# Kernel tuning notes

Hardware: AMD Instinct MI355X
Metric: run time of the kernel (lower is better)

Reference implementation:

```python
import jax, jax.numpy as jnp
import numpy as np

B, N, D = 4, 2048, 1024
H = 16
HD = D // H          # 64
SCALE = 1.0 / HD     # module uses 1/head_dim (NOT 1/sqrt)
NEG = -10000.0       # masked_fill value used by the module
THETA = 10000.0


def setup_inputs() -> dict:
    key = jax.random.key(0)
    ks = jax.random.split(key, 6)
    s = (1.0 / D) ** 0.5  # init_method_normal((1/dim)**0.5)
    return {
        "x": jax.random.normal(ks[0], (B, N, D), jnp.float32),
        "Wq": jax.random.normal(ks[1], (D, D), jnp.float32) * s,
        "Wk": jax.random.normal(ks[2], (D, D), jnp.float32) * s,
        "Wv": jax.random.normal(ks[3], (D, D), jnp.float32) * s,
        "Wo": jax.random.normal(ks[4], (D, D), jnp.float32) * s,
        "bo": jnp.zeros((D,), jnp.float32),
    }


def _rope(t):
    # t: [b, h, n, d]; interleaved-pair rotary (lucidrains rotate_queries_or_keys)
    d, n = t.shape[-1], t.shape[-2]
    inv_freq = 1.0 / (THETA ** (jnp.arange(0, d, 2, dtype=jnp.float32) / d))  # [d/2]
    ang = jnp.arange(n, dtype=jnp.float32)[:, None] * inv_freq[None, :]        # [n, d/2]
    cos = jnp.repeat(jnp.cos(ang), 2, axis=-1)  # [n, d]
    sin = jnp.repeat(jnp.sin(ang), 2, axis=-1)
    x1, x2 = t[..., ::2], t[..., 1::2]
    rot = jnp.stack([-x2, x1], axis=-1).reshape(t.shape)  # rotate_half
    return t * cos + rot * sin


def reference(x, Wq, Wk, Wv, Wo, bo):
    b, n, _ = x.shape
    # QKV projections (no bias; torch Linear: x @ W.T)
    q = (x @ Wq.T).reshape(b, n, H, HD).transpose(0, 2, 1, 3)  # [b,h,n,d]
    k = (x @ Wk.T).reshape(b, n, H, HD).transpose(0, 2, 1, 3)
    v = (x @ Wv.T).reshape(b, n, H, HD).transpose(0, 2, 1, 3)
    # RoPE on q, k
    q = _rope(q)
    k = _rope(k)
    # additive mask: 0 on/below diagonal, -10000 above (causal_mask=True path)
    i = jnp.arange(n)
    add_mask = jnp.where(i[:, None] >= i[None, :], 0.0, NEG).astype(x.dtype)  # [n,n]
    scores = jnp.einsum("bhqd,bhkd->bhqk", q, k) * SCALE + add_mask
    attn = jax.nn.softmax(scores, axis=-1)
    out = jnp.einsum("bhqk,bhkd->bhqd", attn, v)            # [b,h,n,d]
    out = out.transpose(0, 2, 1, 3).reshape(b, n, H * HD)    # [b,n,D]
    return out @ Wo.T + bo
```

## Files before the change

### kernel.cpp

```cpp
#include <hip/hip_runtime.h>
#include <hip/hip_bf16.h>
#include <math.h>

#define B_ 4
#define N_ 2048
#define D_ 1024
#define H_ 16
#define HD_ 64
#define SCALE_ 0.015625f
#define MD_ ((size_t)B_ * N_ * D_)
#define DD_ ((size_t)D_ * D_)
#define BHSZ_ ((size_t)N_ * HD_)
#define QSC_ 0.0225421143f

typedef __hip_bfloat16 bf16;
typedef __attribute__((ext_vector_type(8))) __bf16 bf16x8;
typedef __attribute__((ext_vector_type(4))) float f32x4;
typedef __attribute__((ext_vector_type(16))) float f32x16;

__device__ __forceinline__ float b2f(bf16 x) { return __bfloat162float(x); }
__device__ __forceinline__ bf16 f2b(float x) { return __float2bfloat16(x); }

__device__ __forceinline__ unsigned int pk2(float a, float b) {
  union { bf16 h[2]; unsigned int u; } t;
  t.h[0] = f2b(a); t.h[1] = f2b(b);
  return t.u;
}
__device__ __forceinline__ unsigned int pk2t(float a, float b) {
  return (__float_as_uint(a) >> 16) | (__float_as_uint(b) & 0xffff0000u);
}

__device__ __forceinline__ void gl_lds16(const bf16* g, bf16* l) {
  __builtin_amdgcn_global_load_lds(
      (const __attribute__((address_space(1))) void*)g,
      (__attribute__((address_space(3))) void*)l, 16, 0, 0);
}

__global__ __launch_bounds__(256) void cvt_all(
    const float* __restrict__ x,  const float* __restrict__ wq,
    const float* __restrict__ wk, const float* __restrict__ wv,
    const float* __restrict__ wo, bf16* __restrict__ xb,
    bf16* __restrict__ wb)
{
  const int blk = blockIdx.x;
  const float* s; bf16* d; int i;
  if (blk < 4096)      { s = x;  d = xb;           i = blk; }
  else if (blk < 4608) { s = wq; d = wb;           i = blk - 4096; }
  else if (blk < 5120) { s = wk; d = wb + DD_;     i = blk - 4608; }
  else if (blk < 5632) { s = wv; d = wb + 2 * DD_; i = blk - 5120; }
  else                 { s = wo; d = wb + 3 * DD_; i = blk - 5632; }
  int e = (i * 256 + threadIdx.x) * 8;
  float4 a = *reinterpret_cast<const float4*>(s + e);
  float4 b = *reinterpret_cast<const float4*>(s + e + 4);
  bf16 t[8] = {f2b(a.x), f2b(a.y), f2b(a.z), f2b(a.w),
               f2b(b.x), f2b(b.y), f2b(b.z), f2b(b.w)};
  *reinterpret_cast<int4*>(d + e) = *reinterpret_cast<const int4*>(t);
}

template <int MODE>
__global__ __launch_bounds__(256) void mgemm(
    const bf16* __restrict__ A, const bf16* __restrict__ W,
    const float* __restrict__ bias, void* __restrict__ Cv,
    int M, int N, int K)
{
  __shared__ bf16 As[128 * 32];
  __shared__ bf16 Ws[128 * 32];

  const int tid  = threadIdx.x;
  const int w    = tid >> 6;
  const int lane = tid & 63;
  const int bm   = blockIdx.y * 128;
  const int bn   = blockIdx.x * 128;

  const int wr = (w >> 1) * 64;
  const int wc = (w & 1) * 64;
  const int lm   = lane & 15;
  const int quad = lane >> 4;

  const int srow = lane >> 2;
  const int sslot = (lane & 3) ^ ((lane >> 3) & 3);
  const int scol = sslot * 8;

  const int rsw  = (quad ^ ((lm >> 1) & 3)) * 8;

  f32x4 acc[4][4] = {};

  for (int k0 = 0; k0 < K; k0 += 32) {
#pragma unroll
    for (int cc = 0; cc < 2; ++cc) {
      int c = w * 2 + cc;
      int r = c * 16 + srow;
      gl_lds16(A + (size_t)(bm + r) * K + k0 + scol, &As[c * 512]);
      gl_lds16(W + (size_t)(bn + r) * K + k0 + scol, &Ws[c * 512]);
    }
    __syncthreads();

    bf16x8 af[4], bf_[4];
#pragma unroll
    for (int mi = 0; mi < 4; ++mi)
      af[mi] = *reinterpret_cast<const bf16x8*>(&As[(wr + mi * 16 + lm) * 32 + rsw]);
#pragma unroll
    for (int ni = 0; ni < 4; ++ni)
      bf_[ni] = *reinterpret_cast<const bf16x8*>(&Ws[(wc + ni * 16 + lm) * 32 + rsw]);

#pragma unroll
    for (int mi = 0; mi < 4; ++mi)
#pragma unroll
      for (int ni = 0; ni < 4; ++ni)
        acc[mi][ni] = __builtin_amdgcn_mfma_f32_16x16x32_bf16(
            af[mi], bf_[ni], acc[mi][ni], 0, 0, 0);
    __syncthreads();
  }

#pragma unroll
  for (int mi = 0; mi < 4; ++mi) {
#pragma unroll
    for (int r = 0; r < 4; ++r) {
      int row = bm + wr + mi * 16 + quad * 4 + r;
#pragma unroll
      for (int ni = 0; ni < 4; ++ni) {
        int col = bn + wc + ni * 16 + lm;
        float v = acc[mi][ni][r];
        if (MODE == 1) {
          v += bias[col];
          reinterpret_cast<float*>(Cv)[(size_t)row * N + col] = v;
        } else {
          int reg = col >> 10;
          int cc  = col & 1023;
          int bb  = row >> 11;
          int n   = row & (N_ - 1);
          int hh  = cc >> 6;
          int dd  = cc & 63;
          if (reg < 2) {
            int t32 = n >> 5, m = n & 31;
            int s = dd >> 4, hb = (dd >> 3) & 1, j = dd & 7;
            reinterpret_cast<bf16*>(Cv)[(size_t)reg * MD_ +
                (size_t)(bb * H_ + hh) * BHSZ_ +
                (size_t)t32 * 2048 + s * 512 + hb * 256 + m * 8 + j] = f2b(v);
          } else {
            int t32 = n >> 5, kk = n & 31;
            int hf = kk >> 4, hb = (kk >> 3) & 1, j = kk & 7;
            reinterpret_cast<bf16*>(Cv)[2 * MD_ +
                (size_t)(bb * H_ + hh) * BHSZ_ +
                (size_t)t32 * 2048 + hf * 1024 + hb * 512 + dd * 8 + j] = f2b(v);
          }
        }
      }
    }
  }
}

__global__ __launch_bounds__(256) void rope_inplace(bf16* __restrict__ qf,
                                                    bf16* __restrict__ kf)
{
  const int half = blockIdx.x >> 12;
  const int blk  = blockIdx.x & 4095;
  bf16* base = half ? kf : qf;
  const float LN_THETA = 9.210340371976184f;

  size_t e = ((size_t)blk * 256 + threadIdx.x) * 8;
  int within = (int)(e & (BHSZ_ - 1));
  int t32 = within >> 11;
  int rem = within & 2047;
  int s  = rem >> 9;
  int hb = (rem >> 8) & 1;
  int m  = (rem >> 3) & 31;
  int n  = t32 * 32 + m;

  uint4 raw = *reinterpret_cast<const uint4*>(base + e);
  unsigned int pr[4] = {raw.x, raw.y, raw.z, raw.w};
  unsigned int outw[4];
#pragma unroll
  for (int p = 0; p < 4; ++p) {
    int i = s * 8 + hb * 4 + p;
    float inv = __expf(-((float)(2 * i) / (float)HD_) * LN_THETA);
    float ang = (float)n * inv;
    float sv, cv;
    sincosf(ang, &sv, &cv);
    float a = b2f(((bf16*)&pr[p])[0]);
    float c = b2f(((bf16*)&pr[p])[1]);
    float r0 = a * cv - c * sv;
    float r1 = c * cv + a * sv;
    if (half == 0) { r0 *= QSC_; r1 *= QSC_; }
    outw[p] = pk2(r0, r1);
  }
  uint4 o = {outw[0], outw[1], outw[2], outw[3]};
  *reinterpret_cast<uint4*>(base + e) = o;
}

__global__ __launch_bounds__(128) void fattn4_kernel(
    const bf16* __restrict__ Qf, const bf16* __restrict__ Kf,
    const bf16* __restrict__ Vf, bf16* __restrict__ O)
{
  __shared__ float Ls[32 * 64];
  __shared__ float Ll[64];

  const int wv   = threadIdx.x >> 6;
  const int lane = threadIdx.x & 63;
  const int blk  = blockIdx.x;
  const int xcd  = blk & 7;
  const int j    = blk >> 3;
  const int qt   = 63 - (j >> 3);
  const int bh   = xcd * 8 + (j & 7);
  const int b    = bh >> 4;
  const int h    = bh & 15;
  const int col  = lane & 31;
  const int hi   = lane >> 5;

  const bf16* Qb = Qf + (size_t)bh * BHSZ_ + (size_t)qt * 2048 + hi * 256 + col * 8;
  const bf16* Kb = Kf + (size_t)bh * BHSZ_ + hi * 256 + col * 8;
  const bf16* Vb = Vf + (size_t)bh * BHSZ_ + hi * 512 + col * 8;

  bf16x8 qb[4];
#pragma unroll
  for (int s = 0; s < 4; ++s)
    qb[s] = *reinterpret_cast<const bf16x8*>(Qb + s * 512);

  f32x16 o0 = {}, o1 = {};
  float lsum = 0.f;

  for (int kst = wv; kst <= qt; kst += 2) {
    const bf16* kp = Kb + (size_t)kst * 2048;
    f32x16 st = {};
#pragma unroll
    for (int s = 0; s < 4; ++s) {
      bf16x8 ka = *reinterpret_cast<const bf16x8*>(kp + s * 512);
      st = __builtin_amdgcn_mfma_f32_32x32x16_bf16(ka, qb[s], st, 0, 0, 0);
    }

    float pe[16];
    if (kst == qt) {
#pragma unroll
      for (int r = 0; r < 16; ++r) {
        int koff = (r & 3) + 8 * (r >> 2) + 4 * hi;
        float e = (koff <= col) ? exp2f(st[r]) : 0.f;
        pe[r] = e; lsum += e;
      }
    } else {
#pragma unroll
      for (int r = 0; r < 16; ++r) {
        float e = exp2f(st[r]);
        pe[r] = e; lsum += e;
      }
    }

    const bf16* vp = Vb + (size_t)kst * 2048;
#pragma unroll
    for (int hf = 0; hf < 2; ++hf) {
      unsigned int a0 = pk2t(pe[8 * hf + 0], pe[8 * hf + 1]);
      unsigned int a1 = pk2t(pe[8 * hf + 2], pe[8 * hf + 3]);
      unsigned int b0 = pk2t(pe[8 * hf + 4], pe[8 * hf + 5]);
      unsigned int b1 = pk2t(pe[8 * hf + 6], pe[8 * hf + 7]);
      unsigned int s0 = hi ? a0 : b0;
      unsigned int s1 = hi ? a1 : b1;
      unsigned int r0 = (unsigned int)__shfl_xor((int)s0, 32);
      unsigned int r1 = (unsigned int)__shfl_xor((int)s1, 32);
      union { uint4 u; bf16x8 v; } pb;
      pb.u.x = hi ? r0 : a0;
      pb.u.y = hi ? r1 : a1;
      pb.u.z = hi ? b0 : r0;
      pb.u.w = hi ? b1 : r1;

      bf16x8 v0 = *reinterpret_cast<const bf16x8*>(vp + hf * 1024);
      bf16x8 v1 = *reinterpret_cast<const bf16x8*>(vp + hf * 1024 + 256);
      o0 = __builtin_amdgcn_mfma_f32_32x32x16_bf16(v0, pb.v, o0, 0, 0, 0);
      o1 = __builtin_amdgcn_mfma_f32_32x32x16_bf16(v1, pb.v, o1, 0, 0, 0);
    }
  }

  if (wv == 1) {
#pragma unroll
    for (int r = 0; r < 16; ++r) {
      Ls[r * 64 + lane]        = o0[r];
      Ls[(16 + r) * 64 + lane] = o1[r];
    }
    Ll[lane] = lsum;
  }
  __syncthreads();
  if (wv == 0) {
    float lt = lsum + Ll[lane];
    lt += __shfl_xor(lt, 32);
    float inv = 1.f / lt;
#pragma unroll
    for (int r = 0; r < 16; ++r) {
      o0[r] = (o0[r] + Ls[r * 64 + lane]) * inv;
      o1[r] = (o1[r] + Ls[(16 + r) * 64 + lane]) * inv;
    }
    bf16* Op = O + ((size_t)(b * N_ + 32 * qt + col)) * D_ + h * HD_;
#pragma unroll
    for (int g = 0; g < 4; ++g) {
      uint2 u;
      u.x = pk2(o0[4 * g + 0], o0[4 * g + 1]);
      u.y = pk2(o0[4 * g + 2], o0[4 * g + 3]);
      *reinterpret_cast<uint2*>(Op + 8 * g + 4 * hi) = u;
      u.x = pk2(o1[4 * g + 0], o1[4 * g + 1]);
      u.y = pk2(o1[4 * g + 2], o1[4 * g + 3]);
      *reinterpret_cast<uint2*>(Op + 32 + 8 * g + 4 * hi) = u;
    }
  }
}

extern "C" void kernel_launch(void* const* d_in, const int* in_sizes, int n_in,
                              void* d_out, int out_size, void* d_ws, size_t ws_size,
                              hipStream_t stream)
{
  const float* x  = (const float*)d_in[0];
  const float* Wq = (const float*)d_in[1];
  const float* Wk = (const float*)d_in[2];
  const float* Wv = (const float*)d_in[3];
  const float* Wo = (const float*)d_in[4];
  const float* bo = (const float*)d_in[5];
  float* out = (float*)d_out;

  const int M = B_ * N_;

  bf16* xb  = (bf16*)d_ws;
  bf16* qf  = xb + MD_;
  bf16* kf  = qf + MD_;
  bf16* vf  = kf + MD_;
  bf16* Wqb = vf + MD_;
  bf16* Wob = Wqb + 3 * DD_;
  bf16* ao  = xb;

  cvt_all<<<6144, 256, 0, stream>>>(x, Wq, Wk, Wv, Wo, xb, Wqb);

  mgemm<0><<<dim3(24, 64), 256, 0, stream>>>(xb, Wqb, nullptr, qf, M, 3 * D_, D_);

  rope_inplace<<<8192, 256, 0, stream>>>(qf, kf);

  fattn4_kernel<<<4096, 128, 0, stream>>>(qf, kf, vf, ao);

  mgemm<1><<<dim3(8, 64), 256, 0, stream>>>(ao, Wob, bo, out, M, D_, D_);
}
```

Measured before the change: 274.3 us.

## Rewrite projection GEMMs as 8-wave double-buffered pipelined kernel with XCD-aware tile mapping

Replaces the single-buffered 128x128 GEMM with a 512-thread, 256x128 tile kernel that double-buffers K=64 slabs in LDS. Global-to-LDS loads for the next stage are interleaved between MFMA groups, using explicit vmcnt waits, raw barriers and s_setprio. Block IDs are remapped across the 8 XCDs for better L2 locality. This aims to hide load latency and avoid the full sync stall on every K step, at the cost of more LDS, more registers per wave and hand-tuned wait counts that must stay correct.

```diff
diff --git a/kernel.cpp b/kernel.cpp
--- a/kernel.cpp
+++ b/kernel.cpp
@@ -35,6 +35,14 @@
       (const __attribute__((address_space(1))) void*)g,
       (__attribute__((address_space(3))) void*)l, 16, 0, 0);
 }
+
+__device__ __forceinline__ void fbar() {
+  asm volatile("" ::: "memory");
+  __builtin_amdgcn_s_barrier();
+  asm volatile("" ::: "memory");
+}
+
+#define MFMA16(a, b, c) __builtin_amdgcn_mfma_f32_16x16x32_bf16((a), (b), (c), 0, 0, 0)
 
 __global__ __launch_bounds__(256) void cvt_all(
     const float* __restrict__ x,  const float* __restrict__ wq,
@@ -58,68 +66,137 @@
 }
 
 template <int MODE>
-__global__ __launch_bounds__(256) void mgemm(
+__global__ __launch_bounds__(512, 2) void mgemm8(
     const bf16* __restrict__ A, const bf16* __restrict__ W,
     const float* __restrict__ bias, void* __restrict__ Cv,
     int M, int N, int K)
 {
-  __shared__ bf16 As[128 * 32];
-  __shared__ bf16 Ws[128 * 32];
+  __shared__ bf16 As[2 * 2 * 256 * 32];
+  __shared__ bf16 Ws[2 * 2 * 128 * 32];
 
   const int tid  = threadIdx.x;
   const int w    = tid >> 6;
   const int lane = tid & 63;
-  const int bm   = blockIdx.y * 128;
-  const int bn   = blockIdx.x * 128;
-
-  const int wr = (w >> 1) * 64;
-  const int wc = (w & 1) * 64;
+  const int wm   = w >> 2;
+  const int wn   = w & 3;
   const int lm   = lane & 15;
   const int quad = lane >> 4;
 
+  const int wgid = (blockIdx.x & 7) * ((int)gridDim.x >> 3) + ((int)blockIdx.x >> 3);
+  const int nbn  = N >> 7;
+  const int bn   = (wgid % nbn) * 128;
+  const int bm   = (wgid / nbn) * 256;
+
   const int srow = lane >> 2;
-  const int sslot = (lane & 3) ^ ((lane >> 3) & 3);
-  const int scol = sslot * 8;
-
+  const int scol = ((lane & 3) ^ ((lane >> 3) & 3)) * 8;
   const int rsw  = (quad ^ ((lm >> 1) & 3)) * 8;
 
-  f32x4 acc[4][4] = {};
-
-  for (int k0 = 0; k0 < K; k0 += 32) {
-#pragma unroll
-    for (int cc = 0; cc < 2; ++cc) {
-      int c = w * 2 + cc;
-      int r = c * 16 + srow;
-      gl_lds16(A + (size_t)(bm + r) * K + k0 + scol, &As[c * 512]);
-      gl_lds16(W + (size_t)(bn + r) * K + k0 + scol, &Ws[c * 512]);
-    }
-    __syncthreads();
-
-    bf16x8 af[4], bf_[4];
-#pragma unroll
-    for (int mi = 0; mi < 4; ++mi)
-      af[mi] = *reinterpret_cast<const bf16x8*>(&As[(wr + mi * 16 + lm) * 32 + rsw]);
-#pragma unroll
-    for (int ni = 0; ni < 4; ++ni)
-      bf_[ni] = *reinterpret_cast<const bf16x8*>(&Ws[(wc + ni * 16 + lm) * 32 + rsw]);
-
-#pragma unroll
-    for (int mi = 0; mi < 4; ++mi)
-#pragma unroll
-      for (int ni = 0; ni < 4; ++ni)
-        acc[mi][ni] = __builtin_amdgcn_mfma_f32_16x16x32_bf16(
-            af[mi], bf_[ni], acc[mi][ni], 0, 0, 0);
-    __syncthreads();
-  }
-
-#pragma unroll
-  for (int mi = 0; mi < 4; ++mi) {
+  const int NT = K >> 6;
+
+  f32x4 acc[8][2] = {};
+
+  auto ASL = [&](int b, int kh) -> bf16* { return &As[(b * 2 + kh) * 8192]; };
+  auto WSL = [&](int b, int kh) -> bf16* { return &Ws[(b * 2 + kh) * 4096]; };
+
+  auto stA = [&](int b, int kh, int t) {
+    size_t k = (size_t)t * 64 + kh * 32;
+#pragma unroll
+    for (int j = 0; j < 2; ++j) {
+      int c = w * 2 + j;
+      gl_lds16(A + (size_t)(bm + c * 16 + srow) * K + k + scol,
+               ASL(b, kh) + c * 512);
+    }
+  };
+  auto stB = [&](int b, int kh, int t) {
+    size_t k = (size_t)t * 64 + kh * 32;
+    gl_lds16(W + (size_t)(bn + w * 16 + srow) * K + k + scol,
+             WSL(b, kh) + w * 512);
+  };
+
+  auto rdA = [&](const bf16* slab, int mi) -> bf16x8 {
+    return *reinterpret_cast<const bf16x8*>(
+        slab + (wm * 128 + mi * 16 + lm) * 32 + rsw);
+  };
+  auto rdB = [&](const bf16* slab, int ni) -> bf16x8 {
+    return *reinterpret_cast<const bf16x8*>(
+        slab + (wn * 32 + ni * 16 + lm) * 32 + rsw);
+  };
+
+  stA(0, 0, 0); stB(0, 0, 0);
+  stA(0, 1, 0); stB(0, 1, 0);
+  stA(1, 0, 1); stB(1, 0, 1);
+  asm volatile("s_waitcnt vmcnt(3)" ::: "memory");
+  __builtin_amdgcn_s_barrier();
+  asm volatile("" ::: "memory");
+
+#define GROUP(T, S1, S2, WN) do {                                             \
+    const int b_ = (T) & 1;                                                   \
+    const bf16* A0 = ASL(b_, 0); const bf16* A1 = ASL(b_, 1);                 \
+    const bf16* W0 = WSL(b_, 0); const bf16* W1 = WSL(b_, 1);                 \
+    bf16x8 xa[4], yb[2];                                                      \
+                                   \
+    _Pragma("unroll") for (int i = 0; i < 4; ++i) xa[i] = rdA(A0, i);         \
+    _Pragma("unroll") for (int i = 0; i < 2; ++i) yb[i] = rdB(W0, i);         \
+    if (S1) stA(b_ ^ 1, 1, (T) + 1);                                          \
+    fbar();                                                                   \
+    __builtin_amdgcn_s_setprio(1);                                            \
+    _Pragma("unroll") for (int i = 0; i < 4; ++i) {                           \
+      acc[i][0] = MFMA16(xa[i], yb[0], acc[i][0]);                            \
+      acc[i][1] = MFMA16(xa[i], yb[1], acc[i][1]);                            \
+    }                                                                         \
+    __builtin_amdgcn_s_setprio(0);                                            \
+    fbar();                                                                   \
+                            \
+    _Pragma("unroll") for (int i = 0; i < 4; ++i) xa[i] = rdA(A0, 4 + i);     \
+    if (S1) stB(b_ ^ 1, 1, (T) + 1);                                          \
+    fbar();                                                                   \
+    __builtin_amdgcn_s_setprio(1);                                            \
+    _Pragma("unroll") for (int i = 0; i < 4; ++i) {                           \
+      acc[4 + i][0] = MFMA16(xa[i], yb[0], acc[4 + i][0]);                    \
+      acc[4 + i][1] = MFMA16(xa[i], yb[1], acc[4 + i][1]);                    \
+    }                                                                         \
+    __builtin_amdgcn_s_setprio(0);                                            \
+    fbar();                                                                   \
+             \
+    _Pragma("unroll") for (int i = 0; i < 4; ++i) xa[i] = rdA(A1, i);         \
+    _Pragma("unroll") for (int i = 0; i < 2; ++i) yb[i] = rdB(W1, i);         \
+    if (S2) stA(b_, 0, (T) + 2);                                              \
+    fbar();                                                                   \
+    __builtin_amdgcn_s_setprio(1);                                            \
+    _Pragma("unroll") for (int i = 0; i < 4; ++i) {                           \
+      acc[i][0] = MFMA16(xa[i], yb[0], acc[i][0]);                            \
+      acc[i][1] = MFMA16(xa[i], yb[1], acc[i][1]);                            \
+    }                                                                         \
+    __builtin_amdgcn_s_setprio(0);                                            \
+    fbar();                                                                   \
+          \
+    _Pragma("unroll") for (int i = 0; i < 4; ++i) xa[i] = rdA(A1, 4 + i);     \
+    if (S2) stB(b_, 0, (T) + 2);                                              \
+    fbar();                                                                   \
+    __builtin_amdgcn_s_setprio(1);                                            \
+    _Pragma("unroll") for (int i = 0; i < 4; ++i) {                           \
+      acc[4 + i][0] = MFMA16(xa[i], yb[0], acc[4 + i][0]);                    \
+      acc[4 + i][1] = MFMA16(xa[i], yb[1], acc[4 + i][1]);                    \
+    }                                                                         \
+    __builtin_amdgcn_s_setprio(0);                                            \
+    if ((WN) == 3)      asm volatile("s_waitcnt vmcnt(3)" ::: "memory");      \
+    else if ((WN) == 0) asm volatile("s_waitcnt vmcnt(0)" ::: "memory");      \
+    fbar();                                                                   \
+  } while (0)
+
+  for (int t = 0; t < NT - 2; ++t) GROUP(t, true, true, 3);
+  GROUP(NT - 2, true, false, 0);
+  GROUP(NT - 1, false, false, -1);
+#undef GROUP
+
+#pragma unroll
+  for (int mi = 0; mi < 8; ++mi) {
 #pragma unroll
     for (int r = 0; r < 4; ++r) {
-      int row = bm + wr + mi * 16 + quad * 4 + r;
-#pragma unroll
-      for (int ni = 0; ni < 4; ++ni) {
-        int col = bn + wc + ni * 16 + lm;
+      int row = bm + wm * 128 + mi * 16 + quad * 4 + r;
+#pragma unroll
+      for (int ni = 0; ni < 2; ++ni) {
+        int col = bn + wn * 32 + ni * 16 + lm;
         float v = acc[mi][ni][r];
         if (MODE == 1) {
           v += bias[col];
@@ -324,11 +401,11 @@
 
   cvt_all<<<6144, 256, 0, stream>>>(x, Wq, Wk, Wv, Wo, xb, Wqb);
 
-  mgemm<0><<<dim3(24, 64), 256, 0, stream>>>(xb, Wqb, nullptr, qf, M, 3 * D_, D_);
+  mgemm8<0><<<dim3(768), 512, 0, stream>>>(xb, Wqb, nullptr, qf, M, 3 * D_, D_);
 
   rope_inplace<<<8192, 256, 0, stream>>>(qf, kf);
 
   fattn4_kernel<<<4096, 128, 0, stream>>>(qf, kf, vf, ao);
 
-  mgemm<1><<<dim3(8, 64), 256, 0, stream>>>(ao, Wob, bo, out, M, D_, D_);
-}
+  mgemm8<1><<<dim3(256), 512, 0, stream>>>(ao, Wob, bo, out, M, D_, D_);
+}
```

After: 290.6 us. 1.06x slower.

## Replace QKV GEMM with 4-stage LDS ring-buffered 256x192 tile kernel

Applied to the files above, without the earlier changes.

The QKV projection now runs in a dedicated 512-thread kernel. It uses 256x192 tiles and a 4-deep LDS ring of async global-to-LDS loads with partial vmcnt waits and raw barriers. Register fragments are double-buffered so LDS reads overlap MFMA issue, MFMA blocks run at raised priority, and workgroup IDs are remapped for L2 locality. The aim is to hide load latency and cut barrier stalls in the largest GEMM, at the cost of higher LDS use (about 112 KB) and register pressure, which may limit occupancy.

```diff
diff --git a/kernel.cpp b/kernel.cpp
--- a/kernel.cpp
+++ b/kernel.cpp
@@ -35,6 +35,14 @@
       (const __attribute__((address_space(1))) void*)g,
       (__attribute__((address_space(3))) void*)l, 16, 0, 0);
 }
+
+__device__ __forceinline__ void fbar() {
+  asm volatile("" ::: "memory");
+  __builtin_amdgcn_s_barrier();
+  asm volatile("" ::: "memory");
+}
+
+#define MFMA16(a, b, c) __builtin_amdgcn_mfma_f32_16x16x32_bf16((a), (b), (c), 0, 0, 0)
 
 __global__ __launch_bounds__(256) void cvt_all(
     const float* __restrict__ x,  const float* __restrict__ wq,
@@ -57,10 +65,139 @@
   *reinterpret_cast<int4*>(d + e) = *reinterpret_cast<const int4*>(t);
 }
 
-template <int MODE>
-__global__ __launch_bounds__(256) void mgemm(
+__global__ __launch_bounds__(512, 2) void qkv_ring(
     const bf16* __restrict__ A, const bf16* __restrict__ W,
-    const float* __restrict__ bias, void* __restrict__ Cv,
+    bf16* __restrict__ Cv)
+{
+  __shared__ bf16 As[4 * 256 * 32];
+  __shared__ bf16 Ws[4 * 192 * 32];
+
+  const int tid  = threadIdx.x;
+  const int w    = tid >> 6;
+  const int lane = tid & 63;
+  const int wm   = w >> 2;
+  const int wn   = w & 3;
+  const int lm   = lane & 15;
+  const int quad = lane >> 4;
+
+  const int wgid = (blockIdx.x & 7) * 64 + ((int)blockIdx.x >> 3);
+  const int bn   = (wgid & 15) * 192;
+  const int bm   = (wgid >> 4) * 256;
+
+  const int srow = lane >> 2;
+  const int scol = ((lane & 3) ^ ((lane >> 3) & 3)) * 8;
+  const int rsw  = (quad ^ ((lm >> 1) & 3)) * 8;
+
+  f32x4 acc[8][3] = {};
+
+  auto stage = [&](int T) {
+    const int b4 = T & 3;
+    const size_t k0 = (size_t)T * 32;
+    bf16* ab = &As[b4 * 8192];
+    bf16* wb = &Ws[b4 * 6144];
+#pragma unroll
+    for (int j = 0; j < 2; ++j) {
+      int c = 2 * w + j;
+      gl_lds16(A + (size_t)(bm + c * 16 + srow) * 1024 + k0 + scol,
+               ab + c * 512);
+    }
+    if (w < 4) {
+#pragma unroll
+      for (int j = 0; j < 2; ++j) {
+        int c = 2 * w + j;
+        gl_lds16(W + (size_t)(bn + c * 16 + srow) * 1024 + k0 + scol,
+                 wb + c * 512);
+      }
+    } else {
+      int c = 8 + (w - 4);
+      gl_lds16(W + (size_t)(bn + c * 16 + srow) * 1024 + k0 + scol,
+               wb + c * 512);
+    }
+  };
+
+#define RDFR(T1, FA, FB) do {                                                 \
+    const bf16* ab_ = &As[((T1) & 3) * 8192];                                 \
+    const bf16* wb_ = &Ws[((T1) & 3) * 6144];                                 \
+    _Pragma("unroll") for (int mi = 0; mi < 8; ++mi)                          \
+      FA[mi] = *reinterpret_cast<const bf16x8*>(                              \
+          ab_ + (wm * 128 + mi * 16 + lm) * 32 + rsw);                        \
+    _Pragma("unroll") for (int ni = 0; ni < 3; ++ni)                          \
+      FB[ni] = *reinterpret_cast<const bf16x8*>(                              \
+          wb_ + (wn * 48 + ni * 16 + lm) * 32 + rsw);                         \
+  } while (0)
+
+#define MM(FA, FB) do {                                                       \
+    __builtin_amdgcn_s_setprio(1);                                            \
+    _Pragma("unroll") for (int mi = 0; mi < 8; ++mi)                          \
+      _Pragma("unroll") for (int ni = 0; ni < 3; ++ni)                        \
+        acc[mi][ni] = MFMA16(FA[mi], FB[ni], acc[mi][ni]);                    \
+    __builtin_amdgcn_s_setprio(0);                                            \
+  } while (0)
+
+#define WAITN() do {                                                          \
+    if (w < 4) asm volatile("s_waitcnt vmcnt(4)" ::: "memory");               \
+    else       asm volatile("s_waitcnt vmcnt(3)" ::: "memory");               \
+  } while (0)
+
+  bf16x8 fa0[8], fa1[8];
+  bf16x8 fb0[3], fb1[3];
+
+  stage(0); stage(1); stage(2);
+  WAITN();
+  fbar();
+  RDFR(0, fa0, fb0);
+
+  for (int t = 0; t < 28; t += 2) {
+    stage(t + 3); RDFR(t + 1, fa1, fb1); MM(fa0, fb0); WAITN(); fbar();
+    stage(t + 4); RDFR(t + 2, fa0, fb0); MM(fa1, fb1); WAITN(); fbar();
+  }
+  stage(31); RDFR(29, fa1, fb1); MM(fa0, fb0); WAITN(); fbar();
+  RDFR(30, fa0, fb0); MM(fa1, fb1);
+  asm volatile("s_waitcnt vmcnt(0)" ::: "memory");
+  fbar();
+  RDFR(31, fa1, fb1); MM(fa0, fb0);
+  MM(fa1, fb1);
+
+#undef RDFR
+#undef MM
+#undef WAITN
+
+#pragma unroll
+  for (int mi = 0; mi < 8; ++mi) {
+#pragma unroll
+    for (int r = 0; r < 4; ++r) {
+      int row = bm + wm * 128 + mi * 16 + quad * 4 + r;
+#pragma unroll
+      for (int ni = 0; ni < 3; ++ni) {
+        int col = bn + wn * 48 + ni * 16 + lm;
+        float v = acc[mi][ni][r];
+        int reg = col >> 10;
+        int cc  = col & 1023;
+        int bb  = row >> 11;
+        int n   = row & (N_ - 1);
+        int hh  = cc >> 6;
+        int dd  = cc & 63;
+        if (reg < 2) {
+          int t32 = n >> 5, m = n & 31;
+          int s = dd >> 4, hb = (dd >> 3) & 1, j = dd & 7;
+          Cv[(size_t)reg * MD_ +
+             (size_t)(bb * H_ + hh) * BHSZ_ +
+             (size_t)t32 * 2048 + s * 512 + hb * 256 + m * 8 + j] = f2b(v);
+        } else {
+          int t32 = n >> 5, kk = n & 31;
+          int hf = kk >> 4, hb = (kk >> 3) & 1, j = kk & 7;
+          Cv[2 * MD_ +
+             (size_t)(bb * H_ + hh) * BHSZ_ +
+             (size_t)t32 * 2048 + hf * 1024 + hb * 512 + dd * 8 + j] = f2b(v);
+        }
+      }
+    }
+  }
+}
+
+__global__ __launch_bounds__(256) void pgemm(
+    const bf16* __restrict__ A, const bf16* __restrict__ W,
+    const float* __restrict__ bias, float* __restrict__ C,
     int M, int N, int K)
 {
   __shared__ bf16 As[128 * 32];
@@ -80,7 +217,6 @@
   const int srow = lane >> 2;
   const int sslot = (lane & 3) ^ ((lane >> 3) & 3);
   const int scol = sslot * 8;
-
   const int rsw  = (quad ^ ((lm >> 1) & 3)) * 8;
 
   f32x4 acc[4][4] = {};
@@ -120,31 +256,8 @@
 #pragma unroll
       for (int ni = 0; ni < 4; ++ni) {
         int col = bn + wc + ni * 16 + lm;
-        float v = acc[mi][ni][r];
-        if (MODE == 1) {
-          v += bias[col];
-          reinterpret_cast<float*>(Cv)[(size_t)row * N + col] = v;
-        } else {
-          int reg = col >> 10;
-          int cc  = col & 1023;
-          int bb  = row >> 11;
-          int n   = row & (N_ - 1);
-          int hh  = cc >> 6;
-          int dd  = cc & 63;
-          if (reg < 2) {
-            int t32 = n >> 5, m = n & 31;
-            int s = dd >> 4, hb = (dd >> 3) & 1, j = dd & 7;
-            reinterpret_cast<bf16*>(Cv)[(size_t)reg * MD_ +
-                (size_t)(bb * H_ + hh) * BHSZ_ +
-                (size_t)t32 * 2048 + s * 512 + hb * 256 + m * 8 + j] = f2b(v);
-          } else {
-            int t32 = n >> 5, kk = n & 31;
-            int hf = kk >> 4, hb = (kk >> 3) & 1, j = kk & 7;
-            reinterpret_cast<bf16*>(Cv)[2 * MD_ +
-                (size_t)(bb * H_ + hh) * BHSZ_ +
-                (size_t)t32 * 2048 + hf * 1024 + hb * 512 + dd * 8 + j] = f2b(v);
-          }
-        }
+        float v = acc[mi][ni][r] + bias[col];
+        C[(size_t)row * N + col] = v;
       }
     }
   }
@@ -324,11 +437,11 @@
 
   cvt_all<<<6144, 256, 0, stream>>>(x, Wq, Wk, Wv, Wo, xb, Wqb);
 
-  mgemm<0><<<dim3(24, 64), 256, 0, stream>>>(xb, Wqb, nullptr, qf, M, 3 * D_, D_);
+  qkv_ring<<<512, 512, 0, stream>>>(xb, Wqb, qf);
 
   rope_inplace<<<8192, 256, 0, stream>>>(qf, kf);
 
   fattn4_kernel<<<4096, 128, 0, stream>>>(qf, kf, vf, ao);
 
-  mgemm<1><<<dim3(8, 64), 256, 0, stream>>>(ao, Wob, bo, out, M, D_, D_);
-}
+  pgemm<<<dim3(8, 64), 256, 0, stream>>>(ao, Wob, bo, out, M, D_, D_);
+}
```

Result: slower. 282.5 us (+3.0%).

## Fuse RoPE into QKV GEMM epilogue using precomputed cos/sin table

Applied to the files above, without the earlier changes.

Removes the separate rope_inplace kernel, which made an extra read and write pass over the Q and K buffers. RoPE is now applied in the QKV GEMM epilogue: each lane gets its pair partner with a lane shuffle and reads cos/sin from a table built by extra blocks added to the conversion kernel. This saves a kernel launch and the bf16 round trip, at the cost of table lookups and shuffles in the epilogue. Rotation is now done on fp32 accumulators before rounding, which slightly changes numerics.

```diff
diff --git a/kernel.cpp b/kernel.cpp
--- a/kernel.cpp
+++ b/kernel.cpp
@@ -40,9 +40,23 @@
     const float* __restrict__ x,  const float* __restrict__ wq,
     const float* __restrict__ wk, const float* __restrict__ wv,
     const float* __restrict__ wo, bf16* __restrict__ xb,
-    bf16* __restrict__ wb)
+    bf16* __restrict__ wb, float2* __restrict__ rt)
 {
   const int blk = blockIdx.x;
+  if (blk >= 6144) {
+    const float LN_THETA = 9.210340371976184f;
+    int e = ((blk - 6144) * 256 + (int)threadIdx.x) * 4;
+    float fn = (float)(e >> 5);
+#pragma unroll
+    for (int p = 0; p < 4; ++p) {
+      int i = (e & 31) + p;
+      float inv = __expf(-((float)(2 * i) / (float)HD_) * LN_THETA);
+      float sv, cv;
+      sincosf(fn * inv, &sv, &cv);
+      rt[e + p] = make_float2(cv, sv);
+    }
+    return;
+  }
   const float* s; bf16* d; int i;
   if (blk < 4096)      { s = x;  d = xb;           i = blk; }
   else if (blk < 4608) { s = wq; d = wb;           i = blk - 4096; }
@@ -61,7 +75,7 @@
 __global__ __launch_bounds__(256) void mgemm(
     const bf16* __restrict__ A, const bf16* __restrict__ W,
     const float* __restrict__ bias, void* __restrict__ Cv,
-    int M, int N, int K)
+    const float2* __restrict__ rt, int M, int N, int K)
 {
   __shared__ bf16 As[128 * 32];
   __shared__ bf16 Ws[128 * 32];
@@ -131,7 +145,12 @@
           int n   = row & (N_ - 1);
           int hh  = cc >> 6;
           int dd  = cc & 63;
+          float po = __shfl_xor(v, 1);
           if (reg < 2) {
+            float2 cs = rt[(n << 5) + (dd >> 1)];
+            v = (dd & 1) ? (v * cs.x + po * cs.y)
+                         : (v * cs.x - po * cs.y);
+            if (reg == 0) v *= QSC_;
             int t32 = n >> 5, m = n & 31;
             int s = dd >> 4, hb = (dd >> 3) & 1, j = dd & 7;
             reinterpret_cast<bf16*>(Cv)[(size_t)reg * MD_ +
@@ -150,44 +169,6 @@
   }
 }
 
-__global__ __launch_bounds__(256) void rope_inplace(bf16* __restrict__ qf,
-                                                    bf16* __restrict__ kf)
-{
-  const int half = blockIdx.x >> 12;
-  const int blk  = blockIdx.x & 4095;
-  bf16* base = half ? kf : qf;
-  const float LN_THETA = 9.210340371976184f;
-
-  size_t e = ((size_t)blk * 256 + threadIdx.x) * 8;
-  int within = (int)(e & (BHSZ_ - 1));
-  int t32 = within >> 11;
-  int rem = within & 2047;
-  int s  = rem >> 9;
-  int hb = (rem >> 8) & 1;
-  int m  = (rem >> 3) & 31;
-  int n  = t32 * 32 + m;
-
-  uint4 raw = *reinterpret_cast<const uint4*>(base + e);
-  unsigned int pr[4] = {raw.x, raw.y, raw.z, raw.w};
-  unsigned int outw[4];
-#pragma unroll
-  for (int p = 0; p < 4; ++p) {
-    int i = s * 8 + hb * 4 + p;
-    float inv = __expf(-((float)(2 * i) / (float)HD_) * LN_THETA);
-    float ang = (float)n * inv;
-    float sv, cv;
-    sincosf(ang, &sv, &cv);
-    float a = b2f(((bf16*)&pr[p])[0]);
-    float c = b2f(((bf16*)&pr[p])[1]);
-    float r0 = a * cv - c * sv;
-    float r1 = c * cv + a * sv;
-    if (half == 0) { r0 *= QSC_; r1 *= QSC_; }
-    outw[p] = pk2(r0, r1);
-  }
-  uint4 o = {outw[0], outw[1], outw[2], outw[3]};
-  *reinterpret_cast<uint4*>(base + e) = o;
-}
-
 __global__ __launch_bounds__(128) void fattn4_kernel(
     const bf16* __restrict__ Qf, const bf16* __restrict__ Kf,
     const bf16* __restrict__ Vf, bf16* __restrict__ O)
@@ -320,15 +301,14 @@
   bf16* vf  = kf + MD_;
   bf16* Wqb = vf + MD_;
   bf16* Wob = Wqb + 3 * DD_;
+  float2* rt = (float2*)(Wqb + 4 * DD_);
   bf16* ao  = xb;
 
-  cvt_all<<<6144, 256, 0, stream>>>(x, Wq, Wk, Wv, Wo, xb, Wqb);
-
-  mgemm<0><<<dim3(24, 64), 256, 0, stream>>>(xb, Wqb, nullptr, qf, M, 3 * D_, D_);
-
-  rope_inplace<<<8192, 256, 0, stream>>>(qf, kf);
+  cvt_all<<<6208, 256, 0, stream>>>(x, Wq, Wk, Wv, Wo, xb, Wqb, rt);
+
+  mgemm<0><<<dim3(24, 64), 256, 0, stream>>>(xb, Wqb, nullptr, qf, rt, M, 3 * D_, D_);
 
   fattn4_kernel<<<4096, 128, 0, stream>>>(qf, kf, vf, ao);
 
-  mgemm<1><<<dim3(8, 64), 256, 0, stream>>>(ao, Wob, bo, out, M, D_, D_);
-}
+  mgemm<1><<<dim3(8, 64), 256, 0, stream>>>(ao, Wob, bo, out, nullptr, M, D_, D_);
+}
```

Measured after the change: 277.3 us. Within noise of the previous version (+1.1%).
